# Optimization experiments

Hardware: AMD Instinct MI355X
Metric: run time of the kernel (lower is better)

The kernel has to match this reference:

```python
import jax, jax.numpy as jnp
import numpy as np

# Integrator: torchaudio lfilter with a=[1,-1], b=[1,0] ->
#   y[n] = x[n] + y[n-1]  (first-order IIR that is exactly a cumulative sum
#   along the time axis). We implement it directly as a parallel cumsum.

B, C, T = 8, 4, 1048576  # batch, channels, time (~65 s @ 16 kHz)

def setup_inputs() -> dict:
    key = jax.random.key(0)
    x = jax.random.normal(key, (B, C, T), dtype=jnp.float32)
    return {"x": x}

def reference(x):
    # lfilter recursion y[n] = x[n] + y[n-1] == cumulative sum over time axis
    return jnp.cumsum(x, axis=-1)
```

## Files before the change

### kernel.cpp

```cpp
#include <hip/hip_runtime.h>


constexpr int ROWS           = 32;
constexpr int T_LEN          = 1048576;
constexpr int THREADS        = 256;
constexpr int PER_THREAD     = 16;
constexpr int TILE           = THREADS * PER_THREAD;
constexpr int BLOCKS_PER_ROW = T_LEN / TILE;
constexpr int TOTAL_BLOCKS   = ROWS * BLOCKS_PER_ROW;

__global__ __launch_bounds__(THREADS) void integ_phase1(
    const float* __restrict__ x, float* __restrict__ part) {
  const int blk  = blockIdx.x;
  const int row  = blk / BLOCKS_PER_ROW;
  const int tb   = blk % BLOCKS_PER_ROW;
  const size_t base = (size_t)row * T_LEN + (size_t)tb * TILE;
  const float4* p = (const float4*)(x + base);
  const int t = threadIdx.x;

  float s = 0.f;
#pragma unroll
  for (int j = 0; j < 4; ++j) {
    float4 v = p[j * THREADS + t];
    s += (v.x + v.y) + (v.z + v.w);
  }

  const int lane = t & 63;
  const int wid  = t >> 6;
#pragma unroll
  for (int d = 32; d > 0; d >>= 1) s += __shfl_down(s, d, 64);

  __shared__ float wsum[4];
  if (lane == 0) wsum[wid] = s;
  __syncthreads();
  if (t == 0) part[blk] = (wsum[0] + wsum[1]) + (wsum[2] + wsum[3]);
}

__global__ __launch_bounds__(THREADS) void integ_phase2(float* __restrict__ part) {
  const int row = blockIdx.x;
  const int t   = threadIdx.x;
  const int idx = row * BLOCKS_PER_ROW + t;
  const float v = part[idx];

  const int lane = t & 63;
  const int wid  = t >> 6;
  float s = v;
#pragma unroll
  for (int d = 1; d < 64; d <<= 1) {
    float n = __shfl_up(s, d, 64);
    if (lane >= d) s += n;
  }
  __shared__ float wsum[4];
  if (lane == 63) wsum[wid] = s;
  __syncthreads();
  float prev = 0.f;
#pragma unroll
  for (int w = 0; w < 4; ++w) prev += (w < wid) ? wsum[w] : 0.f;

  part[idx] = prev + s - v;
}

__global__ __launch_bounds__(THREADS) void integ_phase3(
    const float* __restrict__ x, float* __restrict__ y,
    const float* __restrict__ part) {
  const int blk  = blockIdx.x;
  const int row  = blk / BLOCKS_PER_ROW;
  const int tb   = blk % BLOCKS_PER_ROW;
  const size_t base = (size_t)row * T_LEN + (size_t)tb * TILE;
  const int t = threadIdx.x;

  const float4* p = (const float4*)(x + base + (size_t)t * PER_THREAD);
  float v[PER_THREAD];
#pragma unroll
  for (int j = 0; j < PER_THREAD / 4; ++j) {
    float4 q = p[j];
    v[4 * j + 0] = q.x; v[4 * j + 1] = q.y; v[4 * j + 2] = q.z; v[4 * j + 3] = q.w;
  }

#pragma unroll
  for (int i = 1; i < PER_THREAD; ++i) v[i] += v[i - 1];
  const float tsum = v[PER_THREAD - 1];

  const int lane = t & 63;
  const int wid  = t >> 6;
  float s = tsum;
#pragma unroll
  for (int d = 1; d < 64; d <<= 1) {
    float n = __shfl_up(s, d, 64);
    if (lane >= d) s += n;
  }
  __shared__ float wsum[4];
  if (lane == 63) wsum[wid] = s;
  __syncthreads();
  float prev = 0.f;
#pragma unroll
  for (int w = 0; w < 4; ++w) prev += (w < wid) ? wsum[w] : 0.f;
  const float ex = prev + s - tsum;

  const float off = part[blk] + ex;
#pragma unroll
  for (int i = 0; i < PER_THREAD; ++i) v[i] += off;

  float4* q = (float4*)(y + base + (size_t)t * PER_THREAD);
#pragma unroll
  for (int j = 0; j < PER_THREAD / 4; ++j) {
    float4 o;
    o.x = v[4 * j + 0]; o.y = v[4 * j + 1]; o.z = v[4 * j + 2]; o.w = v[4 * j + 3];
    q[j] = o;
  }
}

extern "C" void kernel_launch(void* const* d_in, const int* in_sizes, int n_in,
                              void* d_out, int out_size, void* d_ws, size_t ws_size,
                              hipStream_t stream) {
  const float* x = (const float*)d_in[0];
  float* y = (float*)d_out;
  float* part = (float*)d_ws;

  integ_phase1<<<TOTAL_BLOCKS, THREADS, 0, stream>>>(x, part);
  integ_phase2<<<ROWS, THREADS, 0, stream>>>(part);
  integ_phase3<<<TOTAL_BLOCKS, THREADS, 0, stream>>>(x, y, part);
}
```

Measured before the change: 253.3 us.

## Replace three-pass scan with single-pass decoupled lookback scan

Replaces the reduce / scan-partials / rescan pipeline with one kernel using decoupled lookback: blocks take dynamic tile IDs via an atomic ticket, publish aggregate and inclusive-prefix descriptors, and a warp looks back over predecessors to get its offset. This avoids reading the input twice and removes a launch. A small init kernel resets descriptors, and tiles double to 32 elements per thread. Spin-waiting on predecessors adds serialization risk along each row.

```diff
diff --git a/kernel.cpp b/kernel.cpp
--- a/kernel.cpp
+++ b/kernel.cpp
@@ -4,72 +4,36 @@
 constexpr int ROWS           = 32;
 constexpr int T_LEN          = 1048576;
 constexpr int THREADS        = 256;
-constexpr int PER_THREAD     = 16;
+constexpr int PER_THREAD     = 32;
 constexpr int TILE           = THREADS * PER_THREAD;
 constexpr int BLOCKS_PER_ROW = T_LEN / TILE;
 constexpr int TOTAL_BLOCKS   = ROWS * BLOCKS_PER_ROW;
 
-__global__ __launch_bounds__(THREADS) void integ_phase1(
-    const float* __restrict__ x, float* __restrict__ part) {
-  const int blk  = blockIdx.x;
-  const int row  = blk / BLOCKS_PER_ROW;
-  const int tb   = blk % BLOCKS_PER_ROW;
-  const size_t base = (size_t)row * T_LEN + (size_t)tb * TILE;
-  const float4* p = (const float4*)(x + base);
-  const int t = threadIdx.x;
 
-  float s = 0.f;
-#pragma unroll
-  for (int j = 0; j < 4; ++j) {
-    float4 v = p[j * THREADS + t];
-    s += (v.x + v.y) + (v.z + v.w);
-  }
-
-  const int lane = t & 63;
-  const int wid  = t >> 6;
-#pragma unroll
-  for (int d = 32; d > 0; d >>= 1) s += __shfl_down(s, d, 64);
-
-  __shared__ float wsum[4];
-  if (lane == 0) wsum[wid] = s;
-  __syncthreads();
-  if (t == 0) part[blk] = (wsum[0] + wsum[1]) + (wsum[2] + wsum[3]);
+__global__ __launch_bounds__(THREADS) void integ_init(
+    unsigned long long* __restrict__ desc, unsigned int* __restrict__ ticket) {
+  const int i = blockIdx.x * blockDim.x + threadIdx.x;
+  if (i < TOTAL_BLOCKS) desc[i] = 0ULL;
+  if (i == 0) *ticket = 0u;
 }
 
-__global__ __launch_bounds__(THREADS) void integ_phase2(float* __restrict__ part) {
-  const int row = blockIdx.x;
-  const int t   = threadIdx.x;
-  const int idx = row * BLOCKS_PER_ROW + t;
-  const float v = part[idx];
+__global__ __launch_bounds__(THREADS) void integ_scan(
+    const float* __restrict__ x, float* __restrict__ y,
+    unsigned long long* __restrict__ desc, unsigned int* __restrict__ ticket) {
+  __shared__ unsigned int s_bid;
+  __shared__ float s_wsum[4];
+  __shared__ float s_excl;
 
-  const int lane = t & 63;
-  const int wid  = t >> 6;
-  float s = v;
-#pragma unroll
-  for (int d = 1; d < 64; d <<= 1) {
-    float n = __shfl_up(s, d, 64);
-    if (lane >= d) s += n;
-  }
-  __shared__ float wsum[4];
-  if (lane == 63) wsum[wid] = s;
+  const int t = threadIdx.x;
+  if (t == 0) s_bid = atomicAdd(ticket, 1u);
   __syncthreads();
-  float prev = 0.f;
-#pragma unroll
-  for (int w = 0; w < 4; ++w) prev += (w < wid) ? wsum[w] : 0.f;
+  const int bid  = (int)s_bid;
+  const int row  = bid >> 7;
+  const int tile = bid & (BLOCKS_PER_ROW - 1);
+  const size_t base = (size_t)row * T_LEN + (size_t)tile * TILE
+                    + (size_t)t * PER_THREAD;
 
-  part[idx] = prev + s - v;
-}
-
-__global__ __launch_bounds__(THREADS) void integ_phase3(
-    const float* __restrict__ x, float* __restrict__ y,
-    const float* __restrict__ part) {
-  const int blk  = blockIdx.x;
-  const int row  = blk / BLOCKS_PER_ROW;
-  const int tb   = blk % BLOCKS_PER_ROW;
-  const size_t base = (size_t)row * T_LEN + (size_t)tb * TILE;
-  const int t = threadIdx.x;
-
-  const float4* p = (const float4*)(x + base + (size_t)t * PER_THREAD);
+  const float4* p = (const float4*)(x + base);
   float v[PER_THREAD];
 #pragma unroll
   for (int j = 0; j < PER_THREAD / 4; ++j) {
@@ -89,23 +53,87 @@
     float n = __shfl_up(s, d, 64);
     if (lane >= d) s += n;
   }
-  __shared__ float wsum[4];
-  if (lane == 63) wsum[wid] = s;
+  if (lane == 63) s_wsum[wid] = s;
   __syncthreads();
-  float prev = 0.f;
+  float prev = 0.f, agg = 0.f;
 #pragma unroll
-  for (int w = 0; w < 4; ++w) prev += (w < wid) ? wsum[w] : 0.f;
+  for (int w = 0; w < 4; ++w) {
+    const float ws = s_wsum[w];
+    agg += ws;
+    if (w < wid) prev += ws;
+  }
   const float ex = prev + s - tsum;
 
-  const float off = part[blk] + ex;
+  if (wid == 0) {
+    if (tile == 0) {
+      if (lane == 0) {
+        __hip_atomic_store(&desc[bid],
+            (2ULL << 32) | (unsigned long long)__float_as_uint(agg),
+            __ATOMIC_RELAXED, __HIP_MEMORY_SCOPE_AGENT);
+        s_excl = 0.f;
+      }
+    } else {
+      if (lane == 0)
+        __hip_atomic_store(&desc[bid],
+            (1ULL << 32) | (unsigned long long)__float_as_uint(agg),
+            __ATOMIC_RELAXED, __HIP_MEMORY_SCOPE_AGENT);
+
+      float excl   = 0.f;
+      int remaining = tile;
+      int winEnd    = bid;
+      while (remaining > 0) {
+        const int  nwin   = remaining < 64 ? remaining : 64;
+        const bool active = lane < nwin;
+        const int  j      = winEnd - 1 - lane;
+        unsigned long long d = 0ULL;
+        int lp;
+        while (true) {
+          if (active)
+            d = __hip_atomic_load(&desc[j], __ATOMIC_RELAXED,
+                                  __HIP_MEMORY_SCOPE_AGENT);
+          const unsigned st = (unsigned)(d >> 32);
+          const unsigned long long pm = __ballot(active && st == 2u);
+          const unsigned long long zm = __ballot(active && st == 0u);
+          if (pm) {
+            lp = (int)(__ffsll((unsigned long long)pm) - 1);
+            const unsigned long long need =
+                (lp == 0) ? 0ULL : ((1ULL << lp) - 1ULL);
+            if ((zm & need) == 0ULL) break;
+          } else if (zm == 0ULL) {
+            lp = nwin;
+            break;
+          }
+        }
+        float c = 0.f;
+        if (active && lane <= lp)
+          c = __uint_as_float((unsigned)(d & 0xffffffffULL));
+#pragma unroll
+        for (int o = 32; o > 0; o >>= 1) c += __shfl_xor(c, o, 64);
+        excl += c;
+        if (lp < nwin) { remaining = 0; }
+        else           { remaining -= nwin; winEnd -= nwin; }
+      }
+
+      if (lane == 0) {
+        __hip_atomic_store(&desc[bid],
+            (2ULL << 32) | (unsigned long long)__float_as_uint(excl + agg),
+            __ATOMIC_RELAXED, __HIP_MEMORY_SCOPE_AGENT);
+        s_excl = excl;
+      }
+    }
+  }
+  __syncthreads();
+
+  const float off = s_excl + ex;
 #pragma unroll
   for (int i = 0; i < PER_THREAD; ++i) v[i] += off;
 
-  float4* q = (float4*)(y + base + (size_t)t * PER_THREAD);
+  float4* q = (float4*)(y + base);
 #pragma unroll
   for (int j = 0; j < PER_THREAD / 4; ++j) {
     float4 o;
-    o.x = v[4 * j + 0]; o.y = v[4 * j + 1]; o.z = v[4 * j + 2]; o.w = v[4 * j + 3];
+    o.x = v[4 * j + 0]; o.y = v[4 * j + 1];
+    o.z = v[4 * j + 2]; o.w = v[4 * j + 3];
     q[j] = o;
   }
 }
@@ -115,9 +143,9 @@
                               hipStream_t stream) {
   const float* x = (const float*)d_in[0];
   float* y = (float*)d_out;
-  float* part = (float*)d_ws;
+  unsigned long long* desc = (unsigned long long*)d_ws;
+  unsigned int* ticket = (unsigned int*)(desc + TOTAL_BLOCKS);
 
-  integ_phase1<<<TOTAL_BLOCKS, THREADS, 0, stream>>>(x, part);
-  integ_phase2<<<ROWS, THREADS, 0, stream>>>(part);
-  integ_phase3<<<TOTAL_BLOCKS, THREADS, 0, stream>>>(x, y, part);
+  integ_init<<<(TOTAL_BLOCKS + THREADS - 1) / THREADS, THREADS, 0, stream>>>(desc, ticket);
+  integ_scan<<<TOTAL_BLOCKS, THREADS, 0, stream>>>(x, y, desc, ticket);
 }
```

Result: slower. 292.8 us (+15.6%).

## Fold the partial-sum scan into the final scan kernel, dropping a launch

Applied to the files above, without the earlier changes.

Removes the separate single-row scan kernel over block partials. Each block of the final pass now reduces the partials of all earlier blocks in its row itself, using a masked load plus wave and block reductions. This saves one kernel launch and the serial dependency of a tiny 32-block grid. In exchange every block reads up to 256 partials, which is redundant work but cheap and cache-resident.

```diff
diff --git a/kernel.cpp b/kernel.cpp
--- a/kernel.cpp
+++ b/kernel.cpp
@@ -9,24 +9,21 @@
 constexpr int BLOCKS_PER_ROW = T_LEN / TILE;
 constexpr int TOTAL_BLOCKS   = ROWS * BLOCKS_PER_ROW;
 
-__global__ __launch_bounds__(THREADS) void integ_phase1(
+__global__ __launch_bounds__(THREADS) void integ_reduce(
     const float* __restrict__ x, float* __restrict__ part) {
-  const int blk  = blockIdx.x;
-  const int row  = blk / BLOCKS_PER_ROW;
-  const int tb   = blk % BLOCKS_PER_ROW;
-  const size_t base = (size_t)row * T_LEN + (size_t)tb * TILE;
+  const int blk = blockIdx.x;
+  const size_t base = (size_t)blk * TILE;
   const float4* p = (const float4*)(x + base);
   const int t = threadIdx.x;
+  const int lane = t & 63;
+  const int wid  = t >> 6;
 
   float s = 0.f;
 #pragma unroll
-  for (int j = 0; j < 4; ++j) {
+  for (int j = 0; j < TILE / 4 / THREADS; ++j) {
     float4 v = p[j * THREADS + t];
     s += (v.x + v.y) + (v.z + v.w);
   }
-
-  const int lane = t & 63;
-  const int wid  = t >> 6;
 #pragma unroll
   for (int d = 32; d > 0; d >>= 1) s += __shfl_down(s, d, 64);
 
@@ -36,40 +33,26 @@
   if (t == 0) part[blk] = (wsum[0] + wsum[1]) + (wsum[2] + wsum[3]);
 }
 
-__global__ __launch_bounds__(THREADS) void integ_phase2(float* __restrict__ part) {
-  const int row = blockIdx.x;
-  const int t   = threadIdx.x;
-  const int idx = row * BLOCKS_PER_ROW + t;
-  const float v = part[idx];
-
+__global__ __launch_bounds__(THREADS) void integ_scan(
+    const float* __restrict__ x, float* __restrict__ y,
+    const float* __restrict__ part) {
+  const int blk = blockIdx.x;
+  const int row = blk >> 8;
+  const int tb  = blk & (BLOCKS_PER_ROW - 1);
+  const int t = threadIdx.x;
   const int lane = t & 63;
   const int wid  = t >> 6;
-  float s = v;
+
+  __shared__ float s_pred[4];
+  __shared__ float s_wscan[4];
+
+  float ps = (t < tb) ? part[(row << 8) + t] : 0.f;
 #pragma unroll
-  for (int d = 1; d < 64; d <<= 1) {
-    float n = __shfl_up(s, d, 64);
-    if (lane >= d) s += n;
-  }
-  __shared__ float wsum[4];
-  if (lane == 63) wsum[wid] = s;
-  __syncthreads();
-  float prev = 0.f;
-#pragma unroll
-  for (int w = 0; w < 4; ++w) prev += (w < wid) ? wsum[w] : 0.f;
+  for (int o = 32; o > 0; o >>= 1) ps += __shfl_xor(ps, o, 64);
+  if (lane == 0) s_pred[wid] = ps;
 
-  part[idx] = prev + s - v;
-}
-
-__global__ __launch_bounds__(THREADS) void integ_phase3(
-    const float* __restrict__ x, float* __restrict__ y,
-    const float* __restrict__ part) {
-  const int blk  = blockIdx.x;
-  const int row  = blk / BLOCKS_PER_ROW;
-  const int tb   = blk % BLOCKS_PER_ROW;
-  const size_t base = (size_t)row * T_LEN + (size_t)tb * TILE;
-  const int t = threadIdx.x;
-
-  const float4* p = (const float4*)(x + base + (size_t)t * PER_THREAD);
+  const size_t base = (size_t)blk * TILE + (size_t)t * PER_THREAD;
+  const float4* p = (const float4*)(x + base);
   float v[PER_THREAD];
 #pragma unroll
   for (int j = 0; j < PER_THREAD / 4; ++j) {
@@ -81,31 +64,30 @@
   for (int i = 1; i < PER_THREAD; ++i) v[i] += v[i - 1];
   const float tsum = v[PER_THREAD - 1];
 
-  const int lane = t & 63;
-  const int wid  = t >> 6;
   float s = tsum;
 #pragma unroll
   for (int d = 1; d < 64; d <<= 1) {
     float n = __shfl_up(s, d, 64);
     if (lane >= d) s += n;
   }
-  __shared__ float wsum[4];
-  if (lane == 63) wsum[wid] = s;
+  if (lane == 63) s_wscan[wid] = s;
   __syncthreads();
+
+  float off = (s_pred[0] + s_pred[1]) + (s_pred[2] + s_pred[3]);
   float prev = 0.f;
 #pragma unroll
-  for (int w = 0; w < 4; ++w) prev += (w < wid) ? wsum[w] : 0.f;
-  const float ex = prev + s - tsum;
+  for (int w = 0; w < 4; ++w) prev += (w < wid) ? s_wscan[w] : 0.f;
+  off += prev + s - tsum;
 
-  const float off = part[blk] + ex;
 #pragma unroll
   for (int i = 0; i < PER_THREAD; ++i) v[i] += off;
 
-  float4* q = (float4*)(y + base + (size_t)t * PER_THREAD);
+  float4* q = (float4*)(y + base);
 #pragma unroll
   for (int j = 0; j < PER_THREAD / 4; ++j) {
     float4 o;
-    o.x = v[4 * j + 0]; o.y = v[4 * j + 1]; o.z = v[4 * j + 2]; o.w = v[4 * j + 3];
+    o.x = v[4 * j + 0]; o.y = v[4 * j + 1];
+    o.z = v[4 * j + 2]; o.w = v[4 * j + 3];
     q[j] = o;
   }
 }
@@ -117,7 +99,6 @@
   float* y = (float*)d_out;
   float* part = (float*)d_ws;
 
-  integ_phase1<<<TOTAL_BLOCKS, THREADS, 0, stream>>>(x, part);
-  integ_phase2<<<ROWS, THREADS, 0, stream>>>(part);
-  integ_phase3<<<TOTAL_BLOCKS, THREADS, 0, stream>>>(x, y, part);
+  integ_reduce<<<TOTAL_BLOCKS, THREADS, 0, stream>>>(x, part);
+  integ_scan  <<<TOTAL_BLOCKS, THREADS, 0, stream>>>(x, y, part);
 }
```

Measured after the change: 252.2 us. Within noise of the previous version (-0.4%).
